# Performance work log

Measured on AMD Instinct MI355X. Metric: run time of the kernel, lower is better.

Reference implementation:

```python
import jax, jax.numpy as jnp
import numpy as np

N_NODES = 50000
N_EDGES = 800000
D_IN, D_HID, D_OUT = 128, 64, 64


def gcn_conv(x, W, b, src, dst, num_nodes):
    """PyG-style GCNConv: add self-loops, symmetric norm, aggregate at target.
    src/dst already include self-loops. x: [N, Din], W: [Din, Dout]."""
    xw = x @ W  # transform first (Din -> Dout), like PyG
    ew = jnp.ones(src.shape[0], dtype=x.dtype)
    deg = jax.ops.segment_sum(ew, dst, num_segments=num_nodes)
    dis = jnp.where(deg > 0, jax.lax.rsqrt(deg), 0.0)  # deg^{-1/2}
    norm = dis[src] * ew * dis[dst]  # [E+N]
    msgs = norm[:, None] * xw[src]  # gather source features
    out = jax.ops.segment_sum(msgs, dst, num_segments=num_nodes)
    return out + b


def setup_inputs() -> dict:
    key = jax.random.key(0)
    ks = jax.random.split(key, 8)
    x = jax.random.normal(ks[0], (N_NODES, D_IN), dtype=jnp.float32)
    edge_index = jax.random.randint(ks[1], (2, N_EDGES), 0, N_NODES, dtype=jnp.int64)
    W1 = jax.random.normal(ks[2], (D_IN, D_HID), dtype=jnp.float32) * (1.0 / np.sqrt(D_IN))
    b1 = jnp.zeros((D_HID,), dtype=jnp.float32)
    W2 = jax.random.normal(ks[3], (D_HID, D_HID), dtype=jnp.float32) * (1.0 / np.sqrt(D_HID))
    b2 = jnp.zeros((D_HID,), dtype=jnp.float32)
    W3 = jax.random.normal(ks[4], (D_HID, D_OUT), dtype=jnp.float32) * (1.0 / np.sqrt(D_HID))
    b3 = jnp.zeros((D_OUT,), dtype=jnp.float32)
    return {"x": x, "edge_index": edge_index, "W1": W1, "b1": b1,
            "W2": W2, "b2": b2, "W3": W3, "b3": b3}


def reference(x, edge_index, W1, b1, W2, b2, W3, b3):
    # Add self-loops once (shared by all layers), as PyG GCNConv does per layer.
    loop = jnp.arange(N_NODES, dtype=edge_index.dtype)
    src = jnp.concatenate([edge_index[0], loop])
    dst = jnp.concatenate([edge_index[1], loop])
    # Layer 1 + ReLU (dropout is identity in eval mode)
    h = gcn_conv(x, W1, b1, src, dst, N_NODES)
    h = jax.nn.relu(h)
    # Layer 2 + ReLU
    h = gcn_conv(h, W2, b2, src, dst, N_NODES)
    h = jax.nn.relu(h)
    # Layer 3 (no activation)
    out = gcn_conv(h, W3, b3, src, dst, N_NODES)
    return out
```

## Files before the change

kernel.cpp:

```cpp
#include <hip/hip_runtime.h>
#include <hip/hip_fp16.h>

#define N_NODES 50000
#define N_PAD   50048
#define N_EDGES 800000
#define E_TOT   (N_EDGES + N_NODES)
#define D_IN    128
#define D_HID   64

#define NB         196
#define EB_CHUNK   4096
#define BIN_BLOCKS 196

typedef __bf16 bf16x8 __attribute__((ext_vector_type(8)));
typedef float  f32x4  __attribute__((ext_vector_type(4)));


template <int K>
__device__ __forceinline__ void pack_w(const float* __restrict__ W,
                                       __bf16* __restrict__ Bh, __bf16* __restrict__ Bl, int i) {
  constexpr int KS = K / 32;
  int j = i & 7, lane = (i >> 3) & 63, rest = i >> 9;
  int ct = rest / KS, ks = rest - ct * KS;
  int k = ks * 32 + ((lane >> 4) << 3) + j;
  int c = ct * 16 + (lane & 15);
  float v = W[k * 64 + c];
  __bf16 hb = (__bf16)v;
  Bh[i] = hb;
  Bl[i] = (__bf16)(v - (float)hb);
}


__global__ __launch_bounds__(256) void k_binc_sw(const int* __restrict__ dst,
                                                 unsigned* __restrict__ blkcnt,
                                                 const float* __restrict__ W1,
                                                 const float* __restrict__ W2,
                                                 const float* __restrict__ W3,
                                                 __bf16* __restrict__ Wh1, __bf16* __restrict__ Wl1,
                                                 __bf16* __restrict__ Wh2, __bf16* __restrict__ Wl2,
                                                 __bf16* __restrict__ Wh3, __bf16* __restrict__ Wl3) {
  __shared__ unsigned lh[256];
  int blk = blockIdx.x, t = threadIdx.x;
  if (blk < BIN_BLOCKS) {
    lh[t] = 0;
    __syncthreads();
    int base = blk * EB_CHUNK;
    int endv = min(base + EB_CHUNK, N_EDGES);
    for (int e = base + t; e < endv; e += 256)
      atomicAdd(&lh[((unsigned)dst[e]) >> 8], 1u);
    __syncthreads();
    blkcnt[blk * 256 + t] = lh[t];
  } else {
    int b = blk - BIN_BLOCKS;
    if (b < 32)      pack_w<D_IN >(W1, Wh1, Wl1, b * 256 + t);
    else if (b < 48) pack_w<D_HID>(W2, Wh2, Wl2, (b - 32) * 256 + t);
    else             pack_w<D_HID>(W3, Wh3, Wl3, (b - 48) * 256 + t);
  }
}


__global__ __launch_bounds__(256) void k_bscan(const unsigned* __restrict__ blkcnt,
                                               unsigned* __restrict__ blkoff,
                                               unsigned* __restrict__ bucket_cnt,
                                               unsigned* __restrict__ bucket_ebase,
                                               unsigned* __restrict__ bucket_cbase,
                                               unsigned* __restrict__ rowptr) {
  __shared__ unsigned se[256], sc[256];
  int t = threadIdx.x;
  unsigned run = 0;
  for (int b = 0; b < BIN_BLOCKS; b++) {
    unsigned c = blkcnt[b * 256 + t];
    blkoff[b * 256 + t] = run;
    run += c;
  }
  bucket_cnt[t] = run;
  unsigned cnt   = (t < NB) ? run : 0u;
  unsigned nodes = (t < NB) ? (unsigned)min(256, N_NODES - t * 256) : 0u;
  unsigned ctot  = cnt + nodes;
  se[t] = cnt; sc[t] = ctot;
  __syncthreads();
  for (int off = 1; off < 256; off <<= 1) {
    unsigned a = (t >= off) ? se[t - off] : 0u;
    unsigned b = (t >= off) ? sc[t - off] : 0u;
    __syncthreads();
    se[t] += a; sc[t] += b;
    __syncthreads();
  }
  if (t < NB) {
    bucket_ebase[t] = se[t] - cnt;
    bucket_cbase[t] = sc[t] - ctot;
  }
  if (t == 0) rowptr[N_NODES] = E_TOT;
}


__global__ __launch_bounds__(256) void k_bins(const int* __restrict__ src,
                                              const int* __restrict__ dst,
                                              const unsigned* __restrict__ bucket_ebase,
                                              const unsigned* __restrict__ blkoff,
                                              unsigned* __restrict__ temp) {
  __shared__ unsigned lcur[256];
  int blk = blockIdx.x, t = threadIdx.x;
  lcur[t] = bucket_ebase[t] + blkoff[blk * 256 + t];
  __syncthreads();
  int base = blk * EB_CHUNK;
  int endv = min(base + EB_CHUNK, N_EDGES);
  for (int e = base + t; e < endv; e += 256) {
    unsigned d = (unsigned)dst[e];
    unsigned pos = atomicAdd(&lcur[d >> 8], 1u);
    temp[pos] = (unsigned)src[e] | ((d & 255u) << 16);
  }
}


template <int K, bool FIRST>
__device__ __forceinline__ void gemm_body(int bid,
                                          const float* __restrict__ Xf,
                                          const __bf16* __restrict__ Ah,
                                          const __bf16* __restrict__ Al,
                                          const __bf16* __restrict__ Bh,
                                          const __bf16* __restrict__ Bl,
                                          __half* __restrict__ Y) {
  constexpr int KS = K / 32;
  const int tid  = threadIdx.x;
  const int wave = tid >> 6;
  const int lane = tid & 63;
  const int row0 = bid * 64 + wave * 16;
  const int row_a = FIRST ? min(row0 + (lane & 15), N_NODES - 1)
                          : row0 + (lane & 15);
  const int q8 = (lane >> 4) << 3;

  f32x4 acc[4];
#pragma unroll
  for (int ct = 0; ct < 4; ct++) acc[ct] = (f32x4){0.f, 0.f, 0.f, 0.f};

#pragma unroll
  for (int ks = 0; ks < KS; ks++) {
    bf16x8 ah, al;
    if (FIRST) {
      const float4* xr4 = reinterpret_cast<const float4*>(Xf + (size_t)row_a * K);
      float4 f0 = xr4[ks * 8 + (q8 >> 2) + 0];
      float4 f1 = xr4[ks * 8 + (q8 >> 2) + 1];
#pragma unroll
      for (int j = 0; j < 4; j++) {
        float a0 = (&f0.x)[j], a1 = (&f1.x)[j];
        __bf16 h0 = (__bf16)a0, h1 = (__bf16)a1;
        ah[j] = h0;     al[j] = (__bf16)(a0 - (float)h0);
        ah[4 + j] = h1; al[4 + j] = (__bf16)(a1 - (float)h1);
      }
    } else {
      size_t abase = (size_t)row_a * K + q8 + ks * 32;
      ah = *reinterpret_cast<const bf16x8*>(Ah + abase);
      al = *reinterpret_cast<const bf16x8*>(Al + abase);
    }
#pragma unroll
    for (int ct = 0; ct < 4; ct++) {
      bf16x8 bh = *reinterpret_cast<const bf16x8*>(Bh + (size_t)((ct * KS + ks) * 64 + lane) * 8);
      bf16x8 bl = *reinterpret_cast<const bf16x8*>(Bl + (size_t)((ct * KS + ks) * 64 + lane) * 8);
      acc[ct] = __builtin_amdgcn_mfma_f32_16x16x32_bf16(ah, bh, acc[ct], 0, 0, 0);
      acc[ct] = __builtin_amdgcn_mfma_f32_16x16x32_bf16(ah, bl, acc[ct], 0, 0, 0);
      acc[ct] = __builtin_amdgcn_mfma_f32_16x16x32_bf16(al, bh, acc[ct], 0, 0, 0);
    }
  }

  const int rbase = row0 + ((lane >> 4) << 2);
  const int c     = lane & 15;
#pragma unroll
  for (int ct = 0; ct < 4; ct++)
#pragma unroll
    for (int r = 0; r < 4; r++) {
      int row = rbase + r;
      if (row < N_NODES)
        Y[(size_t)row * 64 + ct * 16 + c] = __float2half_rn(acc[ct][r]);
    }
}


__global__ __launch_bounds__(256) void k_csr_gemm1(const unsigned* __restrict__ temp,
                                                   const unsigned* __restrict__ bucket_ebase,
                                                   const unsigned* __restrict__ bucket_cnt,
                                                   const unsigned* __restrict__ bucket_cbase,
                                                   unsigned* __restrict__ rowptr,
                                                   float* __restrict__ dis,
                                                   unsigned short* __restrict__ csr,
                                                   const float* __restrict__ x,
                                                   const __bf16* __restrict__ Wh1,
                                                   const __bf16* __restrict__ Wl1,
                                                   __half* __restrict__ xw) {
  __shared__ unsigned hist[256], sscan[256], lfill[256];
  if (blockIdx.x >= NB) {
    gemm_body<D_IN, true>(blockIdx.x - NB, x, nullptr, nullptr, Wh1, Wl1, xw);
    return;
  }
  int b = blockIdx.x, t = threadIdx.x;
  unsigned ebase = bucket_ebase[b], ecnt = bucket_cnt[b], cbase = bucket_cbase[b];
  int nodes = min(256, N_NODES - b * 256);
  hist[t] = 0;
  __syncthreads();
  for (unsigned i = t; i < ecnt; i += 256)
    atomicAdd(&hist[(temp[ebase + i] >> 16) & 255u], 1u);
  __syncthreads();
  unsigned deg = (t < nodes) ? hist[t] + 1u : 0u;
  sscan[t] = deg;
  __syncthreads();
  for (int off = 1; off < 256; off <<= 1) {
    unsigned v = (t >= off) ? sscan[t - off] : 0u;
    __syncthreads();
    sscan[t] += v;
    __syncthreads();
  }
  unsigned excl = sscan[t] - deg;
  if (t < nodes) {
    int node = b * 256 + t;
    rowptr[node] = cbase + excl;
    dis[node] = rsqrtf((float)deg);
    csr[cbase + excl] = (unsigned short)node;
  }
  lfill[t] = excl + 1u;
  __syncthreads();
  for (unsigned i = t; i < ecnt; i += 256) {
    unsigned v = temp[ebase + i];
    unsigned d = (v >> 16) & 255u;
    unsigned pos = atomicAdd(&lfill[d], 1u);
    csr[cbase + pos] = (unsigned short)(v & 0xFFFFu);
  }
}


__global__ __launch_bounds__(256) void k_gemm23(const __bf16* __restrict__ Ah,
                                                const __bf16* __restrict__ Al,
                                                const __bf16* __restrict__ Bh,
                                                const __bf16* __restrict__ Bl,
                                                __half* __restrict__ Y) {
  gemm_body<D_HID, false>(blockIdx.x, nullptr, Ah, Al, Bh, Bl, Y);
}


template <int MODE>
__global__ __launch_bounds__(256) void k_agg(const float4* __restrict__ XW4,
                                             const unsigned* __restrict__ rowptr,
                                             const unsigned short* __restrict__ csr,
                                             const float* __restrict__ dis,
                                             const float4* __restrict__ bias4,
                                             __bf16* __restrict__ hh,
                                             __bf16* __restrict__ hl,
                                             float4* __restrict__ OUT4) {
  int node = (int)((blockIdx.x * blockDim.x + threadIdx.x) >> 6);
  int lane = threadIdx.x & 63;
  if (node >= N_NODES) return;
  const int sub = lane & 7;
  const int grp = lane >> 3;

  const float disd = dis[node];
  unsigned beg = rowptr[node], end = rowptr[node + 1];
  float acc0[8] = {0,0,0,0,0,0,0,0};
  float acc1[8] = {0,0,0,0,0,0,0,0};

  for (unsigned j = beg; j < end; j += 64) {
    int nj = (int)min(64u, end - j);
    unsigned s = 0u; float nrm = 0.f;
    if (lane < nj) {
      s = csr[j + lane];
      nrm = dis[s] * disd;
    }
    for (int k = 0; k < nj; k += 16) {
      int e0 = k + grp;
      unsigned s0 = (unsigned)__shfl((int)s, e0);
      float    n0 = __shfl(nrm, e0);
      float4 v0 = XW4[(size_t)s0 * 8 + sub];
      const __half2* h0 = reinterpret_cast<const __half2*>(&v0);
#pragma unroll
      for (int q = 0; q < 4; q++) {
        float2 f = __half22float2(h0[q]);
        acc0[2*q]   += n0 * f.x;
        acc0[2*q+1] += n0 * f.y;
      }
      if (k + 8 < nj) {
        int e1 = k + grp + 8;
        unsigned s1 = (unsigned)__shfl((int)s, e1);
        float    n1 = __shfl(nrm, e1);
        float4 v1 = XW4[(size_t)s1 * 8 + sub];
        const __half2* h1 = reinterpret_cast<const __half2*>(&v1);
#pragma unroll
        for (int q = 0; q < 4; q++) {
          float2 f = __half22float2(h1[q]);
          acc1[2*q]   += n1 * f.x;
          acc1[2*q+1] += n1 * f.y;
        }
      }
    }
  }

  float acc[8];
#pragma unroll
  for (int i = 0; i < 8; i++) acc[i] = acc0[i] + acc1[i];
#pragma unroll
  for (int i = 0; i < 8; i++) {
    acc[i] += __shfl_xor(acc[i], 8);
    acc[i] += __shfl_xor(acc[i], 16);
    acc[i] += __shfl_xor(acc[i], 32);
  }

  if (grp == 0) {
    float4 ba = bias4[sub * 2], bb = bias4[sub * 2 + 1];
    acc[0] += ba.x; acc[1] += ba.y; acc[2] += ba.z; acc[3] += ba.w;
    acc[4] += bb.x; acc[5] += bb.y; acc[6] += bb.z; acc[7] += bb.w;
    if (MODE == 0) {
      bf16x8 hv, lv;
#pragma unroll
      for (int i = 0; i < 8; i++) {
        float f = fmaxf(acc[i], 0.f);
        __bf16 hb = (__bf16)f;
        hv[i] = hb;
        lv[i] = (__bf16)(f - (float)hb);
      }
      *reinterpret_cast<bf16x8*>(&hh[(size_t)node * 64 + sub * 8]) = hv;
      *reinterpret_cast<bf16x8*>(&hl[(size_t)node * 64 + sub * 8]) = lv;
    } else {
      float4 o0 = {acc[0], acc[1], acc[2], acc[3]};
      float4 o1 = {acc[4], acc[5], acc[6], acc[7]};
      OUT4[(size_t)node * 16 + sub * 2]     = o0;
      OUT4[(size_t)node * 16 + sub * 2 + 1] = o1;
    }
  }
}


extern "C" void kernel_launch(void* const* d_in, const int* in_sizes, int n_in,
                              void* d_out, int out_size, void* d_ws, size_t ws_size,
                              hipStream_t stream) {
  const float* x    = (const float*)d_in[0];
  const int*   eidx = (const int*)d_in[1];
  const float* W1   = (const float*)d_in[2];
  const float* b1   = (const float*)d_in[3];
  const float* W2   = (const float*)d_in[4];
  const float* b2   = (const float*)d_in[5];
  const float* W3   = (const float*)d_in[6];
  const float* b3   = (const float*)d_in[7];
  float* out = (float*)d_out;

  const int* e_src = eidx;
  const int* e_dst = eidx + N_EDGES;

  size_t off = 0;
  auto alloc = [&](size_t bytes) -> void* {
    void* p = (char*)d_ws + off;
    off += (bytes + 255) & ~(size_t)255;
    return p;
  };
  unsigned*       rowptr = (unsigned*)alloc((size_t)(N_NODES + 1) * 4);
  float*          dis    = (float*)alloc((size_t)N_NODES * 4);
  unsigned short* csr    = (unsigned short*)alloc((size_t)E_TOT * 2);
  unsigned*       temp   = (unsigned*)alloc((size_t)N_EDGES * 4);
  unsigned*       blkcnt = (unsigned*)alloc((size_t)BIN_BLOCKS * 256 * 4);
  unsigned*       blkoff = (unsigned*)alloc((size_t)BIN_BLOCKS * 256 * 4);
  unsigned*       bcnt   = (unsigned*)alloc(256 * 4);
  unsigned*       bebase = (unsigned*)alloc(256 * 4);
  unsigned*       bcbase = (unsigned*)alloc(256 * 4);
  __half*         xw     = (__half*)alloc((size_t)N_PAD * 64 * 2);
  __bf16*         hhA    = (__bf16*)alloc((size_t)N_PAD * 64 * 2);
  __bf16*         hlA    = (__bf16*)alloc((size_t)N_PAD * 64 * 2);
  __bf16*         hhB    = (__bf16*)alloc((size_t)N_PAD * 64 * 2);
  __bf16*         hlB    = (__bf16*)alloc((size_t)N_PAD * 64 * 2);
  __bf16*         Wh1    = (__bf16*)alloc((size_t)D_IN * 64 * 2);
  __bf16*         Wl1    = (__bf16*)alloc((size_t)D_IN * 64 * 2);
  __bf16*         Wh2    = (__bf16*)alloc((size_t)D_HID * 64 * 2);
  __bf16*         Wl2    = (__bf16*)alloc((size_t)D_HID * 64 * 2);
  __bf16*         Wh3    = (__bf16*)alloc((size_t)D_HID * 64 * 2);
  __bf16*         Wl3    = (__bf16*)alloc((size_t)D_HID * 64 * 2);

  const int gemm_grid = N_PAD / 64;
  const int agg_grid  = (N_NODES * 64 + 255) / 256;

  k_binc_sw<<<BIN_BLOCKS + 64, 256, 0, stream>>>(e_dst, blkcnt, W1, W2, W3,
                                                 Wh1, Wl1, Wh2, Wl2, Wh3, Wl3);
  k_bscan<<<1, 256, 0, stream>>>(blkcnt, blkoff, bcnt, bebase, bcbase, rowptr);
  k_bins<<<BIN_BLOCKS, 256, 0, stream>>>(e_src, e_dst, bebase, blkoff, temp);
  k_csr_gemm1<<<NB + gemm_grid, 256, 0, stream>>>(temp, bebase, bcnt, bcbase,
                                                  rowptr, dis, csr, x, Wh1, Wl1, xw);
  k_agg<0><<<agg_grid, 256, 0, stream>>>((const float4*)xw, rowptr, csr, dis,
                                         (const float4*)b1, hhA, hlA, nullptr);
  k_gemm23<<<gemm_grid, 256, 0, stream>>>(hhA, hlA, Wh2, Wl2, xw);
  k_agg<0><<<agg_grid, 256, 0, stream>>>((const float4*)xw, rowptr, csr, dis,
                                         (const float4*)b2, hhB, hlB, nullptr);
  k_gemm23<<<gemm_grid, 256, 0, stream>>>(hhB, hlB, Wh3, Wl3, xw);
  k_agg<1><<<agg_grid, 256, 0, stream>>>((const float4*)xw, rowptr, csr, dis,
                                         (const float4*)b3, nullptr, nullptr, (float4*)out);
}
```

Measured before the change: 139.2 us.

## Replace exact bucket scan with fixed-stride buckets and global atomic fill

The separate count, scan and scatter kernels become one binning kernel. Each block counts its edges per destination bucket in shared memory, then reserves space with a global atomicAdd into a fixed-capacity slot per bucket (ESTRIDE). Because CSR segments are no longer contiguous, a rowend array replaces rowptr[node+1]. This drops two launches and the serial single-block scan. The cost is that correctness depends on no bucket ever holding more than ESTRIDE edges, and the edge order inside each bucket is now nondeterministic.

New measurement: 137.4 us. No clear change (-1.2%).

```diff
diff --git a/kernel.cpp b/kernel.cpp
--- a/kernel.cpp
+++ b/kernel.cpp
@@ -4,13 +4,14 @@
 #define N_NODES 50000
 #define N_PAD   50048
 #define N_EDGES 800000
-#define E_TOT   (N_EDGES + N_NODES)
 #define D_IN    128
 #define D_HID   64
 
 #define NB         196
 #define EB_CHUNK   4096
 #define BIN_BLOCKS 196
+#define ESTRIDE    4864
+#define CSTRIDE    (ESTRIDE + 256)
 
 typedef __bf16 bf16x8 __attribute__((ext_vector_type(8)));
 typedef float  f32x4  __attribute__((ext_vector_type(4)));
@@ -31,80 +32,35 @@
 }
 
 
-__global__ __launch_bounds__(256) void k_binc_sw(const int* __restrict__ dst,
-                                                 unsigned* __restrict__ blkcnt,
+__global__ __launch_bounds__(256) void k_bins_sw(const int* __restrict__ src,
+                                                 const int* __restrict__ dst,
+                                                 unsigned* __restrict__ bucket_fill,
+                                                 unsigned* __restrict__ temp,
                                                  const float* __restrict__ W1,
                                                  const float* __restrict__ W2,
                                                  const float* __restrict__ W3,
                                                  __bf16* __restrict__ Wh1, __bf16* __restrict__ Wl1,
                                                  __bf16* __restrict__ Wh2, __bf16* __restrict__ Wl2,
                                                  __bf16* __restrict__ Wh3, __bf16* __restrict__ Wl3) {
-  __shared__ unsigned lh[256];
+  __shared__ unsigned lh[256], lcur[256];
   int blk = blockIdx.x, t = threadIdx.x;
-  if (blk < BIN_BLOCKS) {
-    lh[t] = 0;
-    __syncthreads();
-    int base = blk * EB_CHUNK;
-    int endv = min(base + EB_CHUNK, N_EDGES);
-    for (int e = base + t; e < endv; e += 256)
-      atomicAdd(&lh[((unsigned)dst[e]) >> 8], 1u);
-    __syncthreads();
-    blkcnt[blk * 256 + t] = lh[t];
-  } else {
+  if (blk >= BIN_BLOCKS) {
     int b = blk - BIN_BLOCKS;
     if (b < 32)      pack_w<D_IN >(W1, Wh1, Wl1, b * 256 + t);
     else if (b < 48) pack_w<D_HID>(W2, Wh2, Wl2, (b - 32) * 256 + t);
     else             pack_w<D_HID>(W3, Wh3, Wl3, (b - 48) * 256 + t);
-  }
-}
-
-
-__global__ __launch_bounds__(256) void k_bscan(const unsigned* __restrict__ blkcnt,
-                                               unsigned* __restrict__ blkoff,
-                                               unsigned* __restrict__ bucket_cnt,
-                                               unsigned* __restrict__ bucket_ebase,
-                                               unsigned* __restrict__ bucket_cbase,
-                                               unsigned* __restrict__ rowptr) {
-  __shared__ unsigned se[256], sc[256];
-  int t = threadIdx.x;
-  unsigned run = 0;
-  for (int b = 0; b < BIN_BLOCKS; b++) {
-    unsigned c = blkcnt[b * 256 + t];
-    blkoff[b * 256 + t] = run;
-    run += c;
-  }
-  bucket_cnt[t] = run;
-  unsigned cnt   = (t < NB) ? run : 0u;
-  unsigned nodes = (t < NB) ? (unsigned)min(256, N_NODES - t * 256) : 0u;
-  unsigned ctot  = cnt + nodes;
-  se[t] = cnt; sc[t] = ctot;
-  __syncthreads();
-  for (int off = 1; off < 256; off <<= 1) {
-    unsigned a = (t >= off) ? se[t - off] : 0u;
-    unsigned b = (t >= off) ? sc[t - off] : 0u;
-    __syncthreads();
-    se[t] += a; sc[t] += b;
-    __syncthreads();
-  }
-  if (t < NB) {
-    bucket_ebase[t] = se[t] - cnt;
-    bucket_cbase[t] = sc[t] - ctot;
-  }
-  if (t == 0) rowptr[N_NODES] = E_TOT;
-}
-
-
-__global__ __launch_bounds__(256) void k_bins(const int* __restrict__ src,
-                                              const int* __restrict__ dst,
-                                              const unsigned* __restrict__ bucket_ebase,
-                                              const unsigned* __restrict__ blkoff,
-                                              unsigned* __restrict__ temp) {
-  __shared__ unsigned lcur[256];
-  int blk = blockIdx.x, t = threadIdx.x;
-  lcur[t] = bucket_ebase[t] + blkoff[blk * 256 + t];
+    return;
+  }
+  lh[t] = 0;
   __syncthreads();
   int base = blk * EB_CHUNK;
   int endv = min(base + EB_CHUNK, N_EDGES);
+  for (int e = base + t; e < endv; e += 256)
+    atomicAdd(&lh[((unsigned)dst[e]) >> 8], 1u);
+  __syncthreads();
+  unsigned c = lh[t];
+  lcur[t] = t * ESTRIDE + (c ? atomicAdd(&bucket_fill[t], c) : 0u);
+  __syncthreads();
   for (int e = base + t; e < endv; e += 256) {
     unsigned d = (unsigned)dst[e];
     unsigned pos = atomicAdd(&lcur[d >> 8], 1u);
@@ -177,10 +133,9 @@
 
 
 __global__ __launch_bounds__(256) void k_csr_gemm1(const unsigned* __restrict__ temp,
-                                                   const unsigned* __restrict__ bucket_ebase,
-                                                   const unsigned* __restrict__ bucket_cnt,
-                                                   const unsigned* __restrict__ bucket_cbase,
+                                                   const unsigned* __restrict__ bucket_fill,
                                                    unsigned* __restrict__ rowptr,
+                                                   unsigned* __restrict__ rowend,
                                                    float* __restrict__ dis,
                                                    unsigned short* __restrict__ csr,
                                                    const float* __restrict__ x,
@@ -193,7 +148,7 @@
     return;
   }
   int b = blockIdx.x, t = threadIdx.x;
-  unsigned ebase = bucket_ebase[b], ecnt = bucket_cnt[b], cbase = bucket_cbase[b];
+  unsigned ebase = b * ESTRIDE, ecnt = bucket_fill[b], cbase = b * CSTRIDE;
   int nodes = min(256, N_NODES - b * 256);
   hist[t] = 0;
   __syncthreads();
@@ -213,6 +168,7 @@
   if (t < nodes) {
     int node = b * 256 + t;
     rowptr[node] = cbase + excl;
+    rowend[node] = cbase + excl + deg;
     dis[node] = rsqrtf((float)deg);
     csr[cbase + excl] = (unsigned short)node;
   }
@@ -239,6 +195,7 @@
 template <int MODE>
 __global__ __launch_bounds__(256) void k_agg(const float4* __restrict__ XW4,
                                              const unsigned* __restrict__ rowptr,
+                                             const unsigned* __restrict__ rowend,
                                              const unsigned short* __restrict__ csr,
                                              const float* __restrict__ dis,
                                              const float4* __restrict__ bias4,
@@ -252,7 +209,7 @@
   const int grp = lane >> 3;
 
   const float disd = dis[node];
-  unsigned beg = rowptr[node], end = rowptr[node + 1];
+  unsigned beg = rowptr[node], end = rowend[node];
   float acc0[8] = {0,0,0,0,0,0,0,0};
   float acc1[8] = {0,0,0,0,0,0,0,0};
 
@@ -348,15 +305,12 @@
     off += (bytes + 255) & ~(size_t)255;
     return p;
   };
-  unsigned*       rowptr = (unsigned*)alloc((size_t)(N_NODES + 1) * 4);
+  unsigned*       rowptr = (unsigned*)alloc((size_t)N_NODES * 4);
+  unsigned*       rowend = (unsigned*)alloc((size_t)N_NODES * 4);
   float*          dis    = (float*)alloc((size_t)N_NODES * 4);
-  unsigned short* csr    = (unsigned short*)alloc((size_t)E_TOT * 2);
-  unsigned*       temp   = (unsigned*)alloc((size_t)N_EDGES * 4);
-  unsigned*       blkcnt = (unsigned*)alloc((size_t)BIN_BLOCKS * 256 * 4);
-  unsigned*       blkoff = (unsigned*)alloc((size_t)BIN_BLOCKS * 256 * 4);
-  unsigned*       bcnt   = (unsigned*)alloc(256 * 4);
-  unsigned*       bebase = (unsigned*)alloc(256 * 4);
-  unsigned*       bcbase = (unsigned*)alloc(256 * 4);
+  unsigned short* csr    = (unsigned short*)alloc((size_t)NB * CSTRIDE * 2);
+  unsigned*       temp   = (unsigned*)alloc((size_t)NB * ESTRIDE * 4);
+  unsigned*       bfill  = (unsigned*)alloc(256 * 4);
   __half*         xw     = (__half*)alloc((size_t)N_PAD * 64 * 2);
   __bf16*         hhA    = (__bf16*)alloc((size_t)N_PAD * 64 * 2);
   __bf16*         hlA    = (__bf16*)alloc((size_t)N_PAD * 64 * 2);
@@ -372,18 +326,17 @@
   const int gemm_grid = N_PAD / 64;
   const int agg_grid  = (N_NODES * 64 + 255) / 256;
 
-  k_binc_sw<<<BIN_BLOCKS + 64, 256, 0, stream>>>(e_dst, blkcnt, W1, W2, W3,
-                                                 Wh1, Wl1, Wh2, Wl2, Wh3, Wl3);
-  k_bscan<<<1, 256, 0, stream>>>(blkcnt, blkoff, bcnt, bebase, bcbase, rowptr);
-  k_bins<<<BIN_BLOCKS, 256, 0, stream>>>(e_src, e_dst, bebase, blkoff, temp);
-  k_csr_gemm1<<<NB + gemm_grid, 256, 0, stream>>>(temp, bebase, bcnt, bcbase,
-                                                  rowptr, dis, csr, x, Wh1, Wl1, xw);
-  k_agg<0><<<agg_grid, 256, 0, stream>>>((const float4*)xw, rowptr, csr, dis,
+  hipMemsetAsync(bfill, 0, 256 * 4, stream);
+  k_bins_sw<<<BIN_BLOCKS + 64, 256, 0, stream>>>(e_src, e_dst, bfill, temp,
+                                                 W1, W2, W3, Wh1, Wl1, Wh2, Wl2, Wh3, Wl3);
+  k_csr_gemm1<<<NB + gemm_grid, 256, 0, stream>>>(temp, bfill, rowptr, rowend,
+                                                  dis, csr, x, Wh1, Wl1, xw);
+  k_agg<0><<<agg_grid, 256, 0, stream>>>((const float4*)xw, rowptr, rowend, csr, dis,
                                          (const float4*)b1, hhA, hlA, nullptr);
   k_gemm23<<<gemm_grid, 256, 0, stream>>>(hhA, hlA, Wh2, Wl2, xw);
-  k_agg<0><<<agg_grid, 256, 0, stream>>>((const float4*)xw, rowptr, csr, dis,
+  k_agg<0><<<agg_grid, 256, 0, stream>>>((const float4*)xw, rowptr, rowend, csr, dis,
                                          (const float4*)b2, hhB, hlB, nullptr);
   k_gemm23<<<gemm_grid, 256, 0, stream>>>(hhB, hlB, Wh3, Wl3, xw);
-  k_agg<1><<<agg_grid, 256, 0, stream>>>((const float4*)xw, rowptr, csr, dis,
+  k_agg<1><<<agg_grid, 256, 0, stream>>>((const float4*)xw, rowptr, rowend, csr, dis,
                                          (const float4*)b3, nullptr, nullptr, (float4*)out);
 }
```
